# Kernel optimization log

Hardware: AMD Instinct MI355X
Metric: run time of the kernel (lower is better)

The kernel has to match this reference:

```python
import jax, jax.numpy as jnp
import numpy as np

N, DIM, K = 65536, 256, 4096

def setup_inputs() -> dict:
    key = jax.random.key(0)
    kx, kc = jax.random.split(key)
    x = jax.random.normal(kx, (N, DIM), dtype=jnp.float32)
    codebook = jax.random.normal(kc, (K, DIM), dtype=jnp.float32) * 0.02
    return {"x": x, "codebook": codebook}

def reference(x, codebook):
    # torch.cdist(x, codebook).argmin(-1) == argmin of squared distances;
    x_sq = jnp.sum(x * x, axis=-1, keepdims=True)           # (n, 1)
    c_sq = jnp.sum(codebook * codebook, axis=-1)            # (k,)
    dots = jnp.einsum('nd,kd->nk', x, codebook)             # (n, k) GEMM
    dist_sq = x_sq - 2.0 * dots + c_sq[None, :]             # (n, k)
    indices = jnp.argmin(dist_sq, axis=-1)                  # (n,)
    quantized = jnp.take(codebook, indices, axis=0)         # (n, dim) gather
    return (quantized, indices)
```

## Files before the change

kernel.cpp:

```cpp
#include <hip/hip_runtime.h>
#include <cfloat>

typedef _Float16 half8 __attribute__((ext_vector_type(8)));
typedef float    f32x4 __attribute__((ext_vector_type(4)));

#define N_ROWS 65536
#define DIM    256
#define KCODES 4096
#define BM 128
#define BN 128
#define BK 32
#define NSLICE (DIM / BK)
#define NCHUNK (KCODES / BN)

#define WS_CSQ 0
#define WS_XSQ 16384
#define WS_CH  278528
#define WS_CL  2375680

#define GLDS(g, l) __builtin_amdgcn_global_load_lds(                       \
    (const __attribute__((address_space(1))) unsigned int*)(g),            \
    (__attribute__((address_space(3))) unsigned int*)(l), 16, 0, 0)

__global__ void prep_codes(const float* __restrict__ cb, float* __restrict__ csq,
                           _Float16* __restrict__ ch, _Float16* __restrict__ cl) {
    int c = blockIdx.x * blockDim.x + threadIdx.x;
    if (c >= KCODES) return;
    const float* row = cb + (size_t)c * DIM;
    float s = 0.f;
    for (int k = 0; k < DIM; k += 4) {
        float4 v = *(const float4*)&row[k];
        s = fmaf(v.x, v.x, s); s = fmaf(v.y, v.y, s);
        s = fmaf(v.z, v.z, s); s = fmaf(v.w, v.w, s);
        float sv[4] = {v.x * 64.f, v.y * 64.f, v.z * 64.f, v.w * 64.f};
        #pragma unroll
        for (int j = 0; j < 4; ++j) {
            _Float16 h = (_Float16)sv[j];
            ch[(size_t)c * DIM + k + j] = h;
            cl[(size_t)c * DIM + k + j] = (_Float16)(sv[j] - (float)h);
        }
    }
    csq[c] = s;
}

__global__ void prep_xsq(const float* __restrict__ x, float* __restrict__ xsq,
                         char* __restrict__ xq) {
    __shared__ float  As[32 * DIM];
    __shared__ double dtmp[128];
    const int t = threadIdx.x;
    const int n0 = blockIdx.x * 32;
    #pragma unroll
    for (int i = 0; i < 8; ++i) {
        int r = 4 * i + (t >> 6), d4 = (t & 63) * 4;
        *(float4*)&As[r * DIM + d4] = *(const float4*)&x[(size_t)(n0 + r) * DIM + d4];
    }
    __syncthreads();
    {
        const int r = t >> 3;
        const int col8 = (t & 7) * 8;
        char* dst = xq + (((size_t)(n0 + r)) << 10) + (size_t)(col8 * 2);
        const float* src = &As[r * DIM + col8];
        #pragma unroll
        for (int i = 0; i < 4; ++i) {
            half8 hv, lv;
            #pragma unroll
            for (int j = 0; j < 8; ++j) {
                float v = src[i * 64 + j];
                _Float16 h = (_Float16)v;
                hv[j] = h;
                lv[j] = (_Float16)(v - (float)h);
            }
            *(half8*)(dst + i * 128) = hv;
            *(half8*)(dst + 512 + i * 128) = lv;
        }
    }
    if (t < 128) {
        int r = t >> 2, part = t & 3;
        const float* ap = &As[r * DIM + 64 * part];
        double s = 0.0;
        for (int k = 0; k < 64; ++k) { double v = (double)ap[k]; s = fma(v, v, s); }
        dtmp[t] = s;
    }
    __syncthreads();
    if (t < 32)
        xsq[n0 + t] = (float)((dtmp[4*t] + dtmp[4*t+1]) + (dtmp[4*t+2] + dtmp[4*t+3]));
}

__global__ __launch_bounds__(256, 2)
void vq_mfma(const float* __restrict__ cb,
             const float* __restrict__ csq, const float* __restrict__ xsq,
             const _Float16* __restrict__ ch, const _Float16* __restrict__ cl,
             float* out_q, float* __restrict__ out_idx) {
    __shared__ _Float16 AhS[2 * BM * BK], AlS[2 * BM * BK];
    __shared__ _Float16 BhS[2 * BN * BK], BlS[2 * BN * BK];

    const int t = threadIdx.x;
    const int lane = t & 63, wave = t >> 6;
    const int wy = wave >> 1, wx = wave & 1;
    const int m = lane & 15, q = lane >> 4;
    const int n0 = blockIdx.x * BM;
    const int swz = (q ^ (m & 3)) * 8;

    const int rq  = lane >> 2;
    const int gph = lane & 3;
    const int glogB = ((gph ^ (rq & 3)) << 4);
    const char* xqb = (const char*)out_q;
    const char* aBase  = xqb + (((size_t)(n0 + wave * 32 + rq)) << 10) + glogB;
    const char* bBaseH = (const char*)ch + (((size_t)(wave * 32 + rq)) << 9) + glogB;
    const char* bBaseL = (const char*)cl + (((size_t)(wave * 32 + rq)) << 9) + glogB;

#define STAGE(ck2, sl2, nb) do {                                             \
    const char* a_  = aBase  + (size_t)((sl2) * 64);                         \
    const size_t bo_ = ((size_t)(ck2) << 16) + (size_t)((sl2) * 64);         \
    const char* bh_ = bBaseH + bo_;                                          \
    const char* bl_ = bBaseL + bo_;                                          \
    _Float16* Ah_ = AhS + (nb) * (BM * BK) + wave * (32 * BK);               \
    _Float16* Al_ = AlS + (nb) * (BM * BK) + wave * (32 * BK);               \
    _Float16* Bh_ = BhS + (nb) * (BN * BK) + wave * (32 * BK);               \
    _Float16* Bl_ = BlS + (nb) * (BN * BK) + wave * (32 * BK);               \
    GLDS(a_,           Ah_);                                                 \
    GLDS(a_ + 16384,   Ah_ + 16 * BK);                                       \
    GLDS(a_ + 512,     Al_);                                                 \
    GLDS(a_ + 16896,   Al_ + 16 * BK);                                       \
    GLDS(bh_,          Bh_);                                                 \
    GLDS(bh_ + 8192,   Bh_ + 16 * BK);                                       \
    GLDS(bl_,          Bl_);                                                 \
    GLDS(bl_ + 8192,   Bl_ + 16 * BK);                                       \
} while (0)

    int aoffs[4], boffs[4];
    #pragma unroll
    for (int tr = 0; tr < 4; ++tr) aoffs[tr] = (64 * wy + 16 * tr + m) * BK + swz;
    #pragma unroll
    for (int tc = 0; tc < 4; ++tc) boffs[tc] = (64 * wx + 16 * tc + m) * BK + swz;

    float xsq_r[16];
    #pragma unroll
    for (int s = 0; s < 16; ++s)
        xsq_r[s] = xsq[n0 + 64 * wy + 16 * (s >> 2) + 4 * q + (s & 3)];

    float best[16]; int bidx[16];
    #pragma unroll
    for (int s = 0; s < 16; ++s) { best[s] = FLT_MAX; bidx[s] = 0; }

    STAGE(0, 0, 0);
    asm volatile("s_waitcnt vmcnt(0)" ::: "memory");
    __syncthreads();

    for (int chunk = 0; chunk < NCHUNK; ++chunk) {
        const int c0 = chunk * BN;
        float csq_c[4];
        #pragma unroll
        for (int tc = 0; tc < 4; ++tc) csq_c[tc] = csq[c0 + 64 * wx + 16 * tc + m];

        f32x4 acc[4][4];
        #pragma unroll
        for (int tr = 0; tr < 4; ++tr)
            #pragma unroll
            for (int tc = 0; tc < 4; ++tc) acc[tr][tc] = (f32x4){0.f, 0.f, 0.f, 0.f};

        #pragma unroll
        for (int sl = 0; sl < NSLICE; ++sl) {
            if (sl < NSLICE - 1) {
                STAGE(chunk, sl + 1, (sl + 1) & 1);
            } else if (chunk < NCHUNK - 1) {
                STAGE(chunk + 1, 0, 0);
            }
            const int cbuf = sl & 1;
            const _Float16* Ahr = AhS + cbuf * (BM * BK);
            const _Float16* Alr = AlS + cbuf * (BM * BK);
            const _Float16* Bhr = BhS + cbuf * (BN * BK);
            const _Float16* Blr = BlS + cbuf * (BN * BK);

            half8 aH[4], aL[4], bH[4], bL[4];
            #pragma unroll
            for (int tr = 0; tr < 4; ++tr) {
                aH[tr] = *(const half8*)&Ahr[aoffs[tr]];
                aL[tr] = *(const half8*)&Alr[aoffs[tr]];
            }
            #pragma unroll
            for (int tc = 0; tc < 4; ++tc) {
                bH[tc] = *(const half8*)&Bhr[boffs[tc]];
                bL[tc] = *(const half8*)&Blr[boffs[tc]];
            }
            #pragma unroll
            for (int tc = 0; tc < 4; ++tc)
                #pragma unroll
                for (int tr = 0; tr < 4; ++tr)
                    acc[tr][tc] = __builtin_amdgcn_mfma_f32_16x16x32_f16(aH[tr], bH[tc], acc[tr][tc], 0, 0, 0);
            #pragma unroll
            for (int tc = 0; tc < 4; ++tc)
                #pragma unroll
                for (int tr = 0; tr < 4; ++tr)
                    acc[tr][tc] = __builtin_amdgcn_mfma_f32_16x16x32_f16(aH[tr], bL[tc], acc[tr][tc], 0, 0, 0);
            #pragma unroll
            for (int tc = 0; tc < 4; ++tc)
                #pragma unroll
                for (int tr = 0; tr < 4; ++tr)
                    acc[tr][tc] = __builtin_amdgcn_mfma_f32_16x16x32_f16(aL[tr], bH[tc], acc[tr][tc], 0, 0, 0);

            if (sl == NSLICE - 1) {
                #pragma unroll
                for (int tc = 0; tc < 4; ++tc) {
                    int c = c0 + 64 * wx + 16 * tc + m;
                    #pragma unroll
                    for (int tr = 0; tr < 4; ++tr) {
                        #pragma unroll
                        for (int e = 0; e < 4; ++e) {
                            float dot = acc[tr][tc][e] * 0.015625f;
                            float d = fmaf(-2.f, dot, xsq_r[tr * 4 + e]) + csq_c[tc];
                            int s = tr * 4 + e;
                            if (d < best[s]) { best[s] = d; bidx[s] = c; }
                        }
                    }
                }
            }
            asm volatile("s_waitcnt vmcnt(0)" ::: "memory");
            __syncthreads();
        }
    }

    #pragma unroll
    for (int s = 0; s < 16; ++s) {
        float v = best[s]; int idx = bidx[s];
        #pragma unroll
        for (int off = 1; off < 16; off <<= 1) {
            float v2 = __shfl_xor(v, off);
            int   i2 = __shfl_xor(idx, off);
            if (v2 < v || (v2 == v && i2 < idx)) { v = v2; idx = i2; }
        }
        best[s] = v; bidx[s] = idx;
    }
    __syncthreads();
    float* rb = (float*)BhS;
    int*   ri = (int*)BlS;
    {
        int s = m;
        int row_local = 64 * wy + 16 * (s >> 2) + 4 * q + (s & 3);
        rb[row_local * 2 + wx] = best[s];
        ri[row_local * 2 + wx] = bidx[s];
    }
    __syncthreads();
    int* widx = (int*)AhS;
    if (t < BM) {
        float d0 = rb[t * 2], d1 = rb[t * 2 + 1];
        int   i0 = ri[t * 2], i1 = ri[t * 2 + 1];
        int w = (d1 < d0 || (d1 == d0 && i1 < i0)) ? i1 : i0;
        widx[t] = w;
        out_idx[n0 + t] = (float)w;
    }
    __syncthreads();
    const int l4 = t & 63, rg = t >> 6;
    #pragma unroll 4
    for (int i = 0; i < 32; ++i) {
        int r = rg + 4 * i;
        *(float4*)&out_q[(size_t)(n0 + r) * DIM + l4 * 4] =
            *(const float4*)&cb[(size_t)widx[r] * DIM + l4 * 4];
    }
#undef STAGE
}

extern "C" void kernel_launch(void* const* d_in, const int* in_sizes, int n_in,
                              void* d_out, int out_size, void* d_ws, size_t ws_size,
                              hipStream_t stream) {
    const float* x  = (const float*)d_in[0];
    const float* cb = (const float*)d_in[1];
    float* out_q   = (float*)d_out;
    float* out_idx = (float*)d_out + (size_t)N_ROWS * DIM;

    float*    csq = (float*)((char*)d_ws + WS_CSQ);
    float*    xsq = (float*)((char*)d_ws + WS_XSQ);
    _Float16* ch  = (_Float16*)((char*)d_ws + WS_CH);
    _Float16* cl  = (_Float16*)((char*)d_ws + WS_CL);

    prep_codes<<<KCODES / 256, 256, 0, stream>>>(cb, csq, ch, cl);
    prep_xsq<<<N_ROWS / 32, 256, 0, stream>>>(x, xsq, (char*)out_q);
    vq_mfma<<<N_ROWS / BM, 256, 0, stream>>>(cb, csq, xsq, ch, cl, out_q, out_idx);
}
```

Measured before the change: 645.7 us.

## Fuse x split/norm prep into main kernel and restage codebook pipeline

Folds the per-row x fp16 hi/lo split and squared-norm computation into the start of the main MFMA kernel. Each block now processes its own 128 rows via LDS and writes the split data to the output scratch, which removes one kernel launch and the xsq workspace round-trip. The codebook prep kernel is rewritten to stage rows through LDS with vectorized half8 stores. The K-loop moves from a full vmcnt(0) drain per slice to issuing the stage two slices ahead into the buffer just consumed, with partial vmcnt waits and raw barriers. This lets the global-to-LDS loads overlap more of the compute, at the cost of added barrier complexity and a serial prep prologue per block.

```diff
diff --git a/kernel.cpp b/kernel.cpp
--- a/kernel.cpp
+++ b/kernel.cpp
@@ -14,7 +14,6 @@
 #define NCHUNK (KCODES / BN)
 
 #define WS_CSQ 0
-#define WS_XSQ 16384
 #define WS_CH  278528
 #define WS_CL  2375680
 
@@ -24,75 +23,52 @@
 
 __global__ void prep_codes(const float* __restrict__ cb, float* __restrict__ csq,
                            _Float16* __restrict__ ch, _Float16* __restrict__ cl) {
-    int c = blockIdx.x * blockDim.x + threadIdx.x;
-    if (c >= KCODES) return;
-    const float* row = cb + (size_t)c * DIM;
-    float s = 0.f;
-    for (int k = 0; k < DIM; k += 4) {
-        float4 v = *(const float4*)&row[k];
-        s = fmaf(v.x, v.x, s); s = fmaf(v.y, v.y, s);
-        s = fmaf(v.z, v.z, s); s = fmaf(v.w, v.w, s);
-        float sv[4] = {v.x * 64.f, v.y * 64.f, v.z * 64.f, v.w * 64.f};
-        #pragma unroll
-        for (int j = 0; j < 4; ++j) {
-            _Float16 h = (_Float16)sv[j];
-            ch[(size_t)c * DIM + k + j] = h;
-            cl[(size_t)c * DIM + k + j] = (_Float16)(sv[j] - (float)h);
-        }
-    }
-    csq[c] = s;
-}
-
-__global__ void prep_xsq(const float* __restrict__ x, float* __restrict__ xsq,
-                         char* __restrict__ xq) {
-    __shared__ float  As[32 * DIM];
-    __shared__ double dtmp[128];
+    __shared__ float As[32 * DIM];
     const int t = threadIdx.x;
-    const int n0 = blockIdx.x * 32;
+    const int c0 = blockIdx.x * 32;
     #pragma unroll
     for (int i = 0; i < 8; ++i) {
         int r = 4 * i + (t >> 6), d4 = (t & 63) * 4;
-        *(float4*)&As[r * DIM + d4] = *(const float4*)&x[(size_t)(n0 + r) * DIM + d4];
+        *(float4*)&As[r * DIM + d4] = *(const float4*)&cb[(size_t)(c0 + r) * DIM + d4];
     }
     __syncthreads();
     {
         const int r = t >> 3;
-        const int col8 = (t & 7) * 8;
-        char* dst = xq + (((size_t)(n0 + r)) << 10) + (size_t)(col8 * 2);
-        const float* src = &As[r * DIM + col8];
+        const int k0 = (t & 7) * 32;
+        const float* src = &As[r * DIM + k0];
+        _Float16* dh = &ch[(size_t)(c0 + r) * DIM + k0];
+        _Float16* dl = &cl[(size_t)(c0 + r) * DIM + k0];
         #pragma unroll
         for (int i = 0; i < 4; ++i) {
             half8 hv, lv;
             #pragma unroll
             for (int j = 0; j < 8; ++j) {
-                float v = src[i * 64 + j];
-                _Float16 h = (_Float16)v;
-                hv[j] = h;
-                lv[j] = (_Float16)(v - (float)h);
-            }
-            *(half8*)(dst + i * 128) = hv;
-            *(half8*)(dst + 512 + i * 128) = lv;
+                float sv = src[i * 8 + j] * 64.f;
+                _Float16 h = (_Float16)sv;
+                hv[j] = h; lv[j] = (_Float16)(sv - (float)h);
+            }
+            *(half8*)(dh + i * 8) = hv;
+            *(half8*)(dl + i * 8) = lv;
         }
     }
-    if (t < 128) {
-        int r = t >> 2, part = t & 3;
-        const float* ap = &As[r * DIM + 64 * part];
-        double s = 0.0;
-        for (int k = 0; k < 64; ++k) { double v = (double)ap[k]; s = fma(v, v, s); }
-        dtmp[t] = s;
-    }
-    __syncthreads();
-    if (t < 32)
-        xsq[n0 + t] = (float)((dtmp[4*t] + dtmp[4*t+1]) + (dtmp[4*t+2] + dtmp[4*t+3]));
+    if (t < 32) {
+        const float* row = &As[t * DIM];
+        float s = 0.f;
+        for (int k = 0; k < DIM; ++k) s = fmaf(row[k], row[k], s);
+        csq[c0 + t] = s;
+    }
 }
 
 __global__ __launch_bounds__(256, 2)
-void vq_mfma(const float* __restrict__ cb,
-             const float* __restrict__ csq, const float* __restrict__ xsq,
+void vq_mfma(const float* __restrict__ x, const float* __restrict__ cb,
+             const float* __restrict__ csq,
              const _Float16* __restrict__ ch, const _Float16* __restrict__ cl,
              float* out_q, float* __restrict__ out_idx) {
-    __shared__ _Float16 AhS[2 * BM * BK], AlS[2 * BM * BK];
-    __shared__ _Float16 BhS[2 * BN * BK], BlS[2 * BN * BK];
+    __shared__ _Float16 LDS[8 * BM * BK];
+    _Float16* AhS = LDS;
+    _Float16* AlS = LDS + 2 * BM * BK;
+    _Float16* BhS = LDS + 4 * BM * BK;
+    _Float16* BlS = LDS + 6 * BM * BK;
 
     const int t = threadIdx.x;
     const int lane = t & 63, wave = t >> 6;
@@ -100,6 +76,62 @@
     const int m = lane & 15, q = lane >> 4;
     const int n0 = blockIdx.x * BM;
     const int swz = (q ^ (m & 3)) * 8;
+
+    {
+        float*  prepF = (float*)LDS;
+        double* dtmp  = (double*)(LDS + 4 * BM * BK);
+        float*  xsqS  = (float*)(LDS + 6 * BM * BK);
+        char*   xqw   = (char*)out_q;
+        for (int g = 0; g < 4; ++g) {
+            const int r0 = g * 32;
+            #pragma unroll
+            for (int i = 0; i < 8; ++i) {
+                int r = 4 * i + (t >> 6), d4 = (t & 63) * 4;
+                *(float4*)&prepF[r * DIM + d4] =
+                    *(const float4*)&x[(size_t)(n0 + r0 + r) * DIM + d4];
+            }
+            __syncthreads();
+            {
+                const int r = t >> 3;
+                const int col8 = (t & 7) * 8;
+                char* dst = xqw + (((size_t)(n0 + r0 + r)) << 10) + (size_t)(col8 * 2);
+                const float* src = &prepF[r * DIM + col8];
+                #pragma unroll
+                for (int i = 0; i < 4; ++i) {
+                    half8 hv, lv;
+                    #pragma unroll
+                    for (int j = 0; j < 8; ++j) {
+                        float v = src[i * 64 + j];
+                        _Float16 h = (_Float16)v;
+                        hv[j] = h; lv[j] = (_Float16)(v - (float)h);
+                    }
+                    *(half8*)(dst + i * 128) = hv;
+                    *(half8*)(dst + 512 + i * 128) = lv;
+                }
+            }
+            if (t < 128) {
+                int r = t >> 2, part = t & 3;
+                const float* ap = &prepF[r * DIM + 64 * part];
+                double s = 0.0;
+                for (int k = 0; k < 64; ++k) { double v = (double)ap[k]; s = fma(v, v, s); }
+                dtmp[t] = s;
+            }
+            __syncthreads();
+            if (t < 32)
+                xsqS[r0 + t] = (float)((dtmp[4*t] + dtmp[4*t+1]) + (dtmp[4*t+2] + dtmp[4*t+3]));
+            __syncthreads();
+        }
+    }
+
+    float xsq_r[16];
+    {
+        const float* xsqS = (const float*)(LDS + 6 * BM * BK);
+        #pragma unroll
+        for (int s = 0; s < 16; ++s)
+            xsq_r[s] = xsqS[64 * wy + 16 * (s >> 2) + 4 * q + (s & 3)];
+    }
+    asm volatile("s_waitcnt vmcnt(0)" ::: "memory");
+    __syncthreads();
 
     const int rq  = lane >> 2;
     const int gph = lane & 3;
@@ -134,18 +166,15 @@
     #pragma unroll
     for (int tc = 0; tc < 4; ++tc) boffs[tc] = (64 * wx + 16 * tc + m) * BK + swz;
 
-    float xsq_r[16];
-    #pragma unroll
-    for (int s = 0; s < 16; ++s)
-        xsq_r[s] = xsq[n0 + 64 * wy + 16 * (s >> 2) + 4 * q + (s & 3)];
-
     float best[16]; int bidx[16];
     #pragma unroll
     for (int s = 0; s < 16; ++s) { best[s] = FLT_MAX; bidx[s] = 0; }
 
     STAGE(0, 0, 0);
-    asm volatile("s_waitcnt vmcnt(0)" ::: "memory");
-    __syncthreads();
+    STAGE(0, 1, 1);
+    asm volatile("s_waitcnt vmcnt(8)" ::: "memory");
+    __builtin_amdgcn_s_barrier();
+    __builtin_amdgcn_sched_barrier(0);
 
     for (int chunk = 0; chunk < NCHUNK; ++chunk) {
         const int c0 = chunk * BN;
@@ -161,11 +190,6 @@
 
         #pragma unroll
         for (int sl = 0; sl < NSLICE; ++sl) {
-            if (sl < NSLICE - 1) {
-                STAGE(chunk, sl + 1, (sl + 1) & 1);
-            } else if (chunk < NCHUNK - 1) {
-                STAGE(chunk + 1, 0, 0);
-            }
             const int cbuf = sl & 1;
             const _Float16* Ahr = AhS + cbuf * (BM * BK);
             const _Float16* Alr = AlS + cbuf * (BM * BK);
@@ -183,6 +207,18 @@
                 bH[tc] = *(const half8*)&Bhr[boffs[tc]];
                 bL[tc] = *(const half8*)&Blr[boffs[tc]];
             }
+
+            const int sl2r = sl + 2;
+            const int ck2 = chunk + (sl2r >> 3);
+            const int sl2 = sl2r & 7;
+            const bool stg = (ck2 < NCHUNK);
+            if (stg) {
+                asm volatile("s_waitcnt lgkmcnt(0)" ::: "memory");
+                __builtin_amdgcn_s_barrier();
+                __builtin_amdgcn_sched_barrier(0);
+                STAGE(ck2, sl2, cbuf);
+            }
+
             #pragma unroll
             for (int tc = 0; tc < 4; ++tc)
                 #pragma unroll
@@ -215,8 +251,13 @@
                     }
                 }
             }
-            asm volatile("s_waitcnt vmcnt(0)" ::: "memory");
-            __syncthreads();
+
+            if (!(chunk == NCHUNK - 1 && sl == NSLICE - 1)) {
+                if (stg) asm volatile("s_waitcnt vmcnt(8)" ::: "memory");
+                else     asm volatile("s_waitcnt vmcnt(0)" ::: "memory");
+                __builtin_amdgcn_s_barrier();
+                __builtin_amdgcn_sched_barrier(0);
+            }
         }
     }
 
@@ -269,11 +310,9 @@
     float* out_idx = (float*)d_out + (size_t)N_ROWS * DIM;
 
     float*    csq = (float*)((char*)d_ws + WS_CSQ);
-    float*    xsq = (float*)((char*)d_ws + WS_XSQ);
     _Float16* ch  = (_Float16*)((char*)d_ws + WS_CH);
     _Float16* cl  = (_Float16*)((char*)d_ws + WS_CL);
 
-    prep_codes<<<KCODES / 256, 256, 0, stream>>>(cb, csq, ch, cl);
-    prep_xsq<<<N_ROWS / 32, 256, 0, stream>>>(x, xsq, (char*)out_q);
-    vq_mfma<<<N_ROWS / BM, 256, 0, stream>>>(cb, csq, xsq, ch, cl, out_q, out_idx);
+    prep_codes<<<KCODES / 32, 256, 0, stream>>>(cb, csq, ch, cl);
+    vq_mfma<<<N_ROWS / BM, 256, 0, stream>>>(x, cb, csq, ch, cl, out_q, out_idx);
 }
```

New measurement: 565.6 us. -12.4%, faster.
